# Kernel tuning notes

Measured on AMD Instinct MI355X. Metric: run time of the kernel, lower is better.

The kernel has to match this reference:

```python
import jax, jax.numpy as jnp
import numpy as np

D = 128
H = 128  # scorer hidden

def setup_inputs() -> dict:
    key = jax.random.key(0)
    ks = jax.random.split(key, 8)
    B, T = 4096, 200
    transformer_out = jax.random.normal(ks[0], (B, T, D), dtype=jnp.float32)
    candidate = jax.random.normal(ks[1], (B, D), dtype=jnp.float32)
    mask = jax.random.randint(ks[2], (B, T), 0, 2).astype(jnp.bool_)
    # scorer params: Linear(3D,H) -> PReLU -> Linear(H,1)
    lim1 = 1.0 / np.sqrt(3 * D)
    W1 = jax.random.uniform(ks[3], (3 * D, H), minval=-lim1, maxval=lim1, dtype=jnp.float32)
    b1 = jax.random.uniform(ks[4], (H,), minval=-lim1, maxval=lim1, dtype=jnp.float32)
    a = jnp.array(0.25, dtype=jnp.float32)  # PReLU default init
    lim2 = 1.0 / np.sqrt(H)
    W2 = jax.random.uniform(ks[5], (H, 1), minval=-lim2, maxval=lim2, dtype=jnp.float32)
    b2 = jax.random.uniform(ks[6], (1,), minval=-lim2, maxval=lim2, dtype=jnp.float32)
    return {"transformer_out": transformer_out, "candidate": candidate, "mask": mask,
            "W1": W1, "b1": b1, "a": a, "W2": W2, "b2": b2}

def reference(transformer_out, candidate, mask, W1, b1, a, W2, b2):
    # transformer_out: [B,T,D], candidate: [B,D]
    cand_exp = jnp.broadcast_to(candidate[:, None, :], transformer_out.shape)  # [B,T,D]
    att_input = jnp.concatenate([transformer_out, cand_exp, transformer_out * cand_exp], axis=-1)  # [B,T,3D]
    h = att_input @ W1 + b1                       # [B,T,H]
    h = jnp.where(h >= 0, h, a * h)               # PReLU (single shared alpha)
    scores = (h @ W2 + b2)[..., 0]                # [B,T]
    scores = jnp.where(mask, scores, -jnp.inf)
    weights = jax.nn.softmax(scores, axis=-1)     # [B,T]
    return jnp.einsum('bt,btd->bd', weights, transformer_out)  # [B,D]
```

## Files before the change

kernel.cpp:

```cpp
#include <hip/hip_runtime.h>
#include <hip/hip_bf16.h>

typedef __attribute__((ext_vector_type(8))) short short8;
typedef __attribute__((ext_vector_type(4))) float f32x4;

#define B_T 200
#define B_D 128

static __device__ __forceinline__ short f2bf(float f) {
  unsigned u = __builtin_bit_cast(unsigned, f);
  u += 0x7fffu + ((u >> 16) & 1u);
  return (short)(u >> 16);
}
static __device__ __forceinline__ short8 cvt8(f32x4 a, f32x4 b) {
  short8 t;
  t[0] = f2bf(a[0]); t[1] = f2bf(a[1]); t[2] = f2bf(a[2]); t[3] = f2bf(a[3]);
  t[4] = f2bf(b[0]); t[5] = f2bf(b[1]); t[6] = f2bf(b[2]); t[7] = f2bf(b[3]);
  return t;
}

__global__ __launch_bounds__(256, 4)
void ta_fused(const float* __restrict__ x,
              const float* __restrict__ cand,
              const void*  __restrict__ maskp,
              const float* __restrict__ W1,
              const float* __restrict__ b1,
              const float* __restrict__ ap,
              const float* __restrict__ W2,
              const float* __restrict__ b2p,
              float* __restrict__ out)
{
  __shared__ __align__(16) short wbt[B_D * B_D];
  __shared__ __align__(16) float part[8][B_D];
  __shared__ float w2_lds[B_D];
  __shared__ float scores[208];
  __shared__ float red[8];

  const int b    = blockIdx.x;
  const int tid  = threadIdx.x;
  const int lane = tid & 63;
  const int wv   = tid >> 6;
  const int l15  = lane & 15;
  const int g    = lane >> 4;

  int flag1b;
  {
    const unsigned char* mb = (const unsigned char*)maskp;
    unsigned long long v8 = *(const unsigned long long*)(mb + lane * 8);
    flag1b = __any((v8 & 0xFFFFFF00FFFFFF00ull) != 0ull);
  }
  bool mk = false;
  if (tid < B_T) {
    if (flag1b) mk = ((const unsigned char*)maskp)[(size_t)b * B_T + tid] != 0;
    else        mk = ((const int*)maskp)[(size_t)b * B_T + tid] != 0;
  }

  if (tid < B_D) w2_lds[tid] = W2[tid];

  const float* cb = cand + (size_t)b * B_D;
  {
    const int j = tid & 127;
    const int h = tid >> 7;
    #pragma unroll 2
    for (int it = 0; it < 8; ++it) {
      const int ko = it * 2 + h;
      const int k0 = ko * 8;
      short8 t;
      #pragma unroll
      for (int e = 0; e < 8; ++e) {
        float c  = cb[k0 + e];
        float wa = W1[(size_t)(k0 + e) * B_D + j];
        float wc = W1[(size_t)(256 + k0 + e) * B_D + j];
        t[e] = f2bf(wa + c * wc);
      }
      *(short8*)&wbt[(ko * B_D + j) * 8] = t;
    }
    float s0 = (h == 0) ? b1[j] : 0.f, s1 = 0.f, s2 = 0.f, s3 = 0.f;
    const float* w1b = W1 + (size_t)(B_D + h * 64) * B_D + j;
    #pragma unroll 8
    for (int k = 0; k < 64; k += 4) {
      s0 = fmaf(cb[h * 64 + k    ], w1b[(size_t)(k    ) * B_D], s0);
      s1 = fmaf(cb[h * 64 + k + 1], w1b[(size_t)(k + 1) * B_D], s1);
      s2 = fmaf(cb[h * 64 + k + 2], w1b[(size_t)(k + 2) * B_D], s2);
      s3 = fmaf(cb[h * 64 + k + 3], w1b[(size_t)(k + 3) * B_D], s3);
    }
    part[h][j] = (s0 + s1) + (s2 + s3);
  }
  __syncthreads();

  float betaL[8], w2L[8];
  #pragma unroll
  for (int nt = 0; nt < 8; ++nt) {
    int col = nt * 16 + l15;
    betaL[nt] = part[0][col] + part[1][col];
    w2L[nt]   = w2_lds[col];
  }
  const float alpha = ap[0];

#define TILE_SCORE(MT) do {                                                   \
    int row = (MT) * 16 + l15; if (row > B_T - 1) row = B_T - 1;              \
    const float* xr = x + ((size_t)b * B_T + row) * B_D + g * 8;              \
    f32x4 p0 = *(const f32x4*)(xr +  0), p1 = *(const f32x4*)(xr +   4);      \
    f32x4 p2 = *(const f32x4*)(xr + 32), p3 = *(const f32x4*)(xr +  36);      \
    f32x4 p4 = *(const f32x4*)(xr + 64), p5 = *(const f32x4*)(xr +  68);      \
    f32x4 p6 = *(const f32x4*)(xr + 96), p7 = *(const f32x4*)(xr + 100);      \
    short8 a0 = cvt8(p0, p1), a1 = cvt8(p2, p3);                              \
    short8 a2 = cvt8(p4, p5), a3 = cvt8(p6, p7);                              \
    float sc[4] = {0.f, 0.f, 0.f, 0.f};                                       \
    _Pragma("unroll")                                                         \
    for (int nt = 0; nt < 8; ++nt) {                                          \
      f32x4 acc = {0.f, 0.f, 0.f, 0.f};                                       \
      const short8* wp = (const short8*)wbt + g * B_D + nt * 16 + l15;        \
      acc = __builtin_amdgcn_mfma_f32_16x16x32_bf16(a0, wp[0],    acc, 0,0,0);\
      acc = __builtin_amdgcn_mfma_f32_16x16x32_bf16(a1, wp[512],  acc, 0,0,0);\
      acc = __builtin_amdgcn_mfma_f32_16x16x32_bf16(a2, wp[1024], acc, 0,0,0);\
      acc = __builtin_amdgcn_mfma_f32_16x16x32_bf16(a3, wp[1536], acc, 0,0,0);\
      _Pragma("unroll")                                                       \
      for (int r = 0; r < 4; ++r) {                                           \
        float h = acc[r] + betaL[nt];                                         \
        float p = (h >= 0.f) ? h : alpha * h;                                 \
        sc[r] += p * w2L[nt];                                                 \
      }                                                                       \
    }                                                                         \
    _Pragma("unroll")                                                         \
    for (int r = 0; r < 4; ++r) {                                             \
      float v = sc[r];                                                        \
      v += __shfl_xor(v, 1, 16); v += __shfl_xor(v, 2, 16);                   \
      v += __shfl_xor(v, 4, 16); v += __shfl_xor(v, 8, 16);                   \
      if (l15 == 0) scores[(MT) * 16 + g * 4 + r] = v;                        \
    }                                                                         \
  } while (0)

  TILE_SCORE(wv);
  TILE_SCORE(4 + wv);
  TILE_SCORE(8 + wv);
  if (wv == 0) TILE_SCORE(12);
#undef TILE_SCORE
  __syncthreads();

  {
    float s = (tid < B_T && mk) ? scores[tid] : -INFINITY;
    float v = s;
    #pragma unroll
    for (int m = 32; m >= 1; m >>= 1) v = fmaxf(v, __shfl_xor(v, m, 64));
    if (lane == 0) red[wv] = v;
    __syncthreads();
    float mx = fmaxf(fmaxf(red[0], red[1]), fmaxf(red[2], red[3]));
    float e = mk ? __expf(s - mx) : 0.f;
    float sv = e;
    #pragma unroll
    for (int m = 32; m >= 1; m >>= 1) sv += __shfl_xor(sv, m, 64);
    if (lane == 0) red[4 + wv] = sv;
    if (tid < 208) scores[tid] = e;
    __syncthreads();
  }

  {
    const int d4 = (tid & 31) << 2;
    const int p  = tid >> 5;
    const float* xc = x + ((size_t)b * B_T + p * 25) * B_D + d4;
    f32x4 acc = {0.f, 0.f, 0.f, 0.f};
    #pragma unroll 5
    for (int t = 0; t < 25; ++t) {
      f32x4 xv = *(const f32x4*)(xc + (size_t)t * B_D);
      float w = scores[p * 25 + t];
      acc[0] = fmaf(w, xv[0], acc[0]);
      acc[1] = fmaf(w, xv[1], acc[1]);
      acc[2] = fmaf(w, xv[2], acc[2]);
      acc[3] = fmaf(w, xv[3], acc[3]);
    }
    __syncthreads();
    *(f32x4*)&part[p][d4] = acc;
  }
  __syncthreads();
  if (tid < B_D) {
    float Z = (red[4] + red[5]) + (red[6] + red[7]);
    float s = 0.f;
    #pragma unroll
    for (int p = 0; p < 8; ++p) s += part[p][tid];
    out[(size_t)b * B_D + tid] = s / Z;
  }
}

extern "C" void kernel_launch(void* const* d_in, const int* in_sizes, int n_in,
                              void* d_out, int out_size, void* d_ws, size_t ws_size,
                              hipStream_t stream) {
  const float* x    = (const float*)d_in[0];
  const float* cand = (const float*)d_in[1];
  const void*  mask = d_in[2];
  const float* W1   = (const float*)d_in[3];
  const float* b1   = (const float*)d_in[4];
  const float* a    = (const float*)d_in[5];
  const float* W2   = (const float*)d_in[6];
  const float* b2   = (const float*)d_in[7];
  float* out = (float*)d_out;
  const int B = in_sizes[1] / B_D;
  ta_fused<<<B, 256, 0, stream>>>(x, cand, mask, W1, b1, a, W2, b2, out);
}
```

Measured before the change: 147.7 us.

## Precompute bf16 W1 fragments and per-batch beta in prep kernels

Adds two prep kernels. One converts the W1 x-part and product-part to bf16 fragments in workspace. The other computes beta = b1 + cand·W1_mid for all batches using an LDS-cached W1 slice. The fused kernel then reads half-size bf16 weight fragments with coalesced 16-byte loads and reads beta directly, instead of re-reading fp32 W1 strided per block. It also aliases the partial-sum buffer onto the weight LDS region, shrinking LDS use, and drops one barrier. The cost is two extra launches and a double bf16 rounding of the folded weights.

```diff
diff --git a/kernel.cpp b/kernel.cpp
--- a/kernel.cpp
+++ b/kernel.cpp
@@ -11,12 +11,62 @@
   unsigned u = __builtin_bit_cast(unsigned, f);
   u += 0x7fffu + ((u >> 16) & 1u);
   return (short)(u >> 16);
+}
+static __device__ __forceinline__ float bf2f(short s) {
+  unsigned u = ((unsigned)(unsigned short)s) << 16;
+  return __builtin_bit_cast(float, u);
 }
 static __device__ __forceinline__ short8 cvt8(f32x4 a, f32x4 b) {
   short8 t;
   t[0] = f2bf(a[0]); t[1] = f2bf(a[1]); t[2] = f2bf(a[2]); t[3] = f2bf(a[3]);
   t[4] = f2bf(b[0]); t[5] = f2bf(b[1]); t[6] = f2bf(b[2]); t[7] = f2bf(b[3]);
   return t;
+}
+
+__global__ __launch_bounds__(256) void ta_prep_w(const float* __restrict__ W1,
+                                                 short* __restrict__ wfrag) {
+  const int o = blockIdx.x * 256 + threadIdx.x;
+  const int j = o & 127, k0 = (o >> 7) * 8;
+  short8 ta, tc;
+  #pragma unroll
+  for (int e = 0; e < 8; ++e) {
+    ta[e] = f2bf(W1[(size_t)(k0 + e) * B_D + j]);
+    tc[e] = f2bf(W1[(size_t)(256 + k0 + e) * B_D + j]);
+  }
+  *(short8*)&wfrag[o * 8] = ta;
+  *(short8*)&wfrag[16384 + o * 8] = tc;
+}
+
+__global__ __launch_bounds__(256) void ta_prep_beta(const float* __restrict__ cand,
+                                                    const float* __restrict__ W1,
+                                                    const float* __restrict__ b1,
+                                                    float* __restrict__ beta, int B) {
+  __shared__ float w1b[B_D][B_D];
+  const int tid = threadIdx.x;
+  #pragma unroll
+  for (int i = 0; i < 16; ++i) {
+    int v = i * 256 + tid;
+    ((f32x4*)w1b)[v] = ((const f32x4*)(W1 + 128 * B_D))[v];
+  }
+  __syncthreads();
+  const int j = tid & 127, which = tid >> 7;
+  const int b0 = blockIdx.x * 8;
+  #pragma unroll
+  for (int bi = 0; bi < 4; ++bi) {
+    int b = b0 + bi * 2 + which;
+    if (b < B) {
+      const float* cb = cand + (size_t)b * B_D;
+      float s0 = b1[j], s1 = 0.f, s2 = 0.f, s3 = 0.f;
+      #pragma unroll 8
+      for (int k = 0; k < 128; k += 4) {
+        s0 = fmaf(cb[k    ], w1b[k    ][j], s0);
+        s1 = fmaf(cb[k + 1], w1b[k + 1][j], s1);
+        s2 = fmaf(cb[k + 2], w1b[k + 2][j], s2);
+        s3 = fmaf(cb[k + 3], w1b[k + 3][j], s3);
+      }
+      beta[(size_t)b * B_D + j] = (s0 + s1) + (s2 + s3);
+    }
+  }
 }
 
 __global__ __launch_bounds__(256, 4)
@@ -27,14 +77,17 @@
               const float* __restrict__ b1,
               const float* __restrict__ ap,
               const float* __restrict__ W2,
-              const float* __restrict__ b2p,
+              const short* __restrict__ wfrag,
+              const float* __restrict__ beta,
+              int use_ws,
               float* __restrict__ out)
 {
   __shared__ __align__(16) short wbt[B_D * B_D];
-  __shared__ __align__(16) float part[8][B_D];
+  __shared__ float bpart[2][B_D];
   __shared__ float w2_lds[B_D];
   __shared__ float scores[208];
   __shared__ float red[8];
+  float (*part)[B_D] = (float (*)[B_D])wbt;
 
   const int b    = blockIdx.x;
   const int tid  = threadIdx.x;
@@ -58,20 +111,31 @@
   if (tid < B_D) w2_lds[tid] = W2[tid];
 
   const float* cb = cand + (size_t)b * B_D;
-  {
-    const int j = tid & 127;
-    const int h = tid >> 7;
+  if (use_ws) {
     #pragma unroll 2
     for (int it = 0; it < 8; ++it) {
-      const int ko = it * 2 + h;
-      const int k0 = ko * 8;
+      const int o = it * 256 + tid;
+      const int k0 = (o >> 7) * 8;
+      short8 wa = *(const short8*)&wfrag[o * 8];
+      short8 wc = *(const short8*)&wfrag[16384 + o * 8];
+      short8 t;
+      #pragma unroll
+      for (int e = 0; e < 8; ++e)
+        t[e] = f2bf(fmaf(cb[k0 + e], bf2f(wc[e]), bf2f(wa[e])));
+      *(short8*)&wbt[o * 8] = t;
+    }
+  } else {
+    const int j = tid & 127, h = tid >> 7;
+    #pragma unroll 2
+    for (int it = 0; it < 8; ++it) {
+      const int ko = it * 2 + h, k0 = ko * 8;
       short8 t;
       #pragma unroll
       for (int e = 0; e < 8; ++e) {
         float c  = cb[k0 + e];
         float wa = W1[(size_t)(k0 + e) * B_D + j];
         float wc = W1[(size_t)(256 + k0 + e) * B_D + j];
-        t[e] = f2bf(wa + c * wc);
+        t[e] = f2bf(fmaf(c, wc, wa));
       }
       *(short8*)&wbt[(ko * B_D + j) * 8] = t;
     }
@@ -84,7 +148,7 @@
       s2 = fmaf(cb[h * 64 + k + 2], w1b[(size_t)(k + 2) * B_D], s2);
       s3 = fmaf(cb[h * 64 + k + 3], w1b[(size_t)(k + 3) * B_D], s3);
     }
-    part[h][j] = (s0 + s1) + (s2 + s3);
+    bpart[h][j] = (s0 + s1) + (s2 + s3);
   }
   __syncthreads();
 
@@ -92,7 +156,7 @@
   #pragma unroll
   for (int nt = 0; nt < 8; ++nt) {
     int col = nt * 16 + l15;
-    betaL[nt] = part[0][col] + part[1][col];
+    betaL[nt] = use_ws ? beta[(size_t)b * B_D + col] : (bpart[0][col] + bpart[1][col]);
     w2L[nt]   = w2_lds[col];
   }
   const float alpha = ap[0];
@@ -169,7 +233,6 @@
       acc[2] = fmaf(w, xv[2], acc[2]);
       acc[3] = fmaf(w, xv[3], acc[3]);
     }
-    __syncthreads();
     *(f32x4*)&part[p][d4] = acc;
   }
   __syncthreads();
@@ -192,8 +255,18 @@
   const float* b1   = (const float*)d_in[4];
   const float* a    = (const float*)d_in[5];
   const float* W2   = (const float*)d_in[6];
-  const float* b2   = (const float*)d_in[7];
   float* out = (float*)d_out;
   const int B = in_sizes[1] / B_D;
-  ta_fused<<<B, 256, 0, stream>>>(x, cand, mask, W1, b1, a, W2, b2, out);
-}
+
+  short* wfrag = (short*)d_ws;
+  float* beta  = (float*)((char*)d_ws + 65536);
+  const size_t need = 65536 + (size_t)B * B_D * sizeof(float);
+  const int use_ws = (ws_size >= need) ? 1 : 0;
+
+  if (use_ws) {
+    ta_prep_w<<<8, 256, 0, stream>>>(W1, wfrag);
+    ta_prep_beta<<<(B + 7) / 8, 256, 0, stream>>>(cand, W1, b1, beta, B);
+  }
+  ta_fused<<<B, 256, 0, stream>>>(x, cand, mask, W1, b1, a, W2,
+                                  wfrag, beta, use_ws, out);
+}
```

New measurement: 152.1 us. 3.0% more time.

## Prefetch x tiles ahead of MFMA scoring and overlap first load with W1 fold

Applied to the files above, without the earlier changes.

Loads the first row tile of x at kernel entry so its latency overlaps the weight-folding prologue. Later tiles are prefetched into registers before computing the current tile's scores. Also reads W2 directly instead of staging it in LDS, uses two accumulators in the weighted pooling loop, and drops a redundant barrier. Occupancy hints change to an explicit waves-per-EU attribute. This raises register pressure in exchange for hiding memory latency.

```diff
diff --git a/kernel.cpp b/kernel.cpp
--- a/kernel.cpp
+++ b/kernel.cpp
@@ -19,7 +19,8 @@
   return t;
 }
 
-__global__ __launch_bounds__(256, 4)
+__global__ __launch_bounds__(256)
+__attribute__((amdgpu_waves_per_eu(4, 4)))
 void ta_fused(const float* __restrict__ x,
               const float* __restrict__ cand,
               const void*  __restrict__ maskp,
@@ -31,8 +32,7 @@
               float* __restrict__ out)
 {
   __shared__ __align__(16) short wbt[B_D * B_D];
-  __shared__ __align__(16) float part[8][B_D];
-  __shared__ float w2_lds[B_D];
+  __shared__ float part[8][B_D];
   __shared__ float scores[208];
   __shared__ float red[8];
 
@@ -43,6 +43,12 @@
   const int l15  = lane & 15;
   const int g    = lane >> 4;
 
+  const float* xr0p = x + ((size_t)b * B_T + wv * 16 + l15) * B_D + g * 8;
+  f32x4 r0 = *(const f32x4*)(xr0p +  0), r1 = *(const f32x4*)(xr0p +   4);
+  f32x4 r2 = *(const f32x4*)(xr0p + 32), r3 = *(const f32x4*)(xr0p +  36);
+  f32x4 r4 = *(const f32x4*)(xr0p + 64), r5 = *(const f32x4*)(xr0p +  68);
+  f32x4 r6 = *(const f32x4*)(xr0p + 96), r7 = *(const f32x4*)(xr0p + 100);
+
   int flag1b;
   {
     const unsigned char* mb = (const unsigned char*)maskp;
@@ -55,23 +61,20 @@
     else        mk = ((const int*)maskp)[(size_t)b * B_T + tid] != 0;
   }
 
-  if (tid < B_D) w2_lds[tid] = W2[tid];
-
   const float* cb = cand + (size_t)b * B_D;
   {
     const int j = tid & 127;
     const int h = tid >> 7;
     #pragma unroll 2
     for (int it = 0; it < 8; ++it) {
-      const int ko = it * 2 + h;
-      const int k0 = ko * 8;
+      const int ko = it * 2 + h, k0 = ko * 8;
       short8 t;
       #pragma unroll
       for (int e = 0; e < 8; ++e) {
         float c  = cb[k0 + e];
         float wa = W1[(size_t)(k0 + e) * B_D + j];
         float wc = W1[(size_t)(256 + k0 + e) * B_D + j];
-        t[e] = f2bf(wa + c * wc);
+        t[e] = f2bf(fmaf(c, wc, wa));
       }
       *(short8*)&wbt[(ko * B_D + j) * 8] = t;
     }
@@ -93,19 +96,19 @@
   for (int nt = 0; nt < 8; ++nt) {
     int col = nt * 16 + l15;
     betaL[nt] = part[0][col] + part[1][col];
-    w2L[nt]   = w2_lds[col];
+    w2L[nt]   = W2[col];
   }
   const float alpha = ap[0];
 
-#define TILE_SCORE(MT) do {                                                   \
-    int row = (MT) * 16 + l15; if (row > B_T - 1) row = B_T - 1;              \
-    const float* xr = x + ((size_t)b * B_T + row) * B_D + g * 8;              \
-    f32x4 p0 = *(const f32x4*)(xr +  0), p1 = *(const f32x4*)(xr +   4);      \
-    f32x4 p2 = *(const f32x4*)(xr + 32), p3 = *(const f32x4*)(xr +  36);      \
-    f32x4 p4 = *(const f32x4*)(xr + 64), p5 = *(const f32x4*)(xr +  68);      \
-    f32x4 p6 = *(const f32x4*)(xr + 96), p7 = *(const f32x4*)(xr + 100);      \
-    short8 a0 = cvt8(p0, p1), a1 = cvt8(p2, p3);                              \
-    short8 a2 = cvt8(p4, p5), a3 = cvt8(p6, p7);                              \
+#define LOADX(MT_ROW) do {                                                    \
+    const float* xp_ = x + ((size_t)b * B_T + (MT_ROW)) * B_D + g * 8;        \
+    r0 = *(const f32x4*)(xp_ +  0); r1 = *(const f32x4*)(xp_ +   4);          \
+    r2 = *(const f32x4*)(xp_ + 32); r3 = *(const f32x4*)(xp_ +  36);          \
+    r4 = *(const f32x4*)(xp_ + 64); r5 = *(const f32x4*)(xp_ +  68);          \
+    r6 = *(const f32x4*)(xp_ + 96); r7 = *(const f32x4*)(xp_ + 100);          \
+  } while (0)
+
+#define COMPUTE_SCORE(TB) do {                                                \
     float sc[4] = {0.f, 0.f, 0.f, 0.f};                                       \
     _Pragma("unroll")                                                         \
     for (int nt = 0; nt < 8; ++nt) {                                          \
@@ -117,9 +120,9 @@
       acc = __builtin_amdgcn_mfma_f32_16x16x32_bf16(a3, wp[1536], acc, 0,0,0);\
       _Pragma("unroll")                                                       \
       for (int r = 0; r < 4; ++r) {                                           \
-        float h = acc[r] + betaL[nt];                                         \
-        float p = (h >= 0.f) ? h : alpha * h;                                 \
-        sc[r] += p * w2L[nt];                                                 \
+        float h_ = acc[r] + betaL[nt];                                        \
+        float p_ = (h_ >= 0.f) ? h_ : alpha * h_;                             \
+        sc[r] += p_ * w2L[nt];                                                \
       }                                                                       \
     }                                                                         \
     _Pragma("unroll")                                                         \
@@ -127,15 +130,31 @@
       float v = sc[r];                                                        \
       v += __shfl_xor(v, 1, 16); v += __shfl_xor(v, 2, 16);                   \
       v += __shfl_xor(v, 4, 16); v += __shfl_xor(v, 8, 16);                   \
-      if (l15 == 0) scores[(MT) * 16 + g * 4 + r] = v;                        \
+      if (l15 == 0) scores[(TB) + g * 4 + r] = v;                             \
     }                                                                         \
   } while (0)
 
-  TILE_SCORE(wv);
-  TILE_SCORE(4 + wv);
-  TILE_SCORE(8 + wv);
-  if (wv == 0) TILE_SCORE(12);
-#undef TILE_SCORE
+  short8 a0 = cvt8(r0, r1), a1 = cvt8(r2, r3), a2 = cvt8(r4, r5), a3 = cvt8(r6, r7);
+  LOADX((4 + wv) * 16 + l15);
+  COMPUTE_SCORE(wv * 16);
+
+  a0 = cvt8(r0, r1); a1 = cvt8(r2, r3); a2 = cvt8(r4, r5); a3 = cvt8(r6, r7);
+  LOADX((8 + wv) * 16 + l15);
+  COMPUTE_SCORE((4 + wv) * 16);
+
+  a0 = cvt8(r0, r1); a1 = cvt8(r2, r3); a2 = cvt8(r4, r5); a3 = cvt8(r6, r7);
+  if (wv == 0) {
+    int row3 = 192 + l15; if (row3 > B_T - 1) row3 = B_T - 1;
+    LOADX(row3);
+  }
+  COMPUTE_SCORE((8 + wv) * 16);
+
+  if (wv == 0) {
+    a0 = cvt8(r0, r1); a1 = cvt8(r2, r3); a2 = cvt8(r4, r5); a3 = cvt8(r6, r7);
+    COMPUTE_SCORE(192);
+  }
+#undef LOADX
+#undef COMPUTE_SCORE
   __syncthreads();
 
   {
@@ -159,18 +178,26 @@
     const int d4 = (tid & 31) << 2;
     const int p  = tid >> 5;
     const float* xc = x + ((size_t)b * B_T + p * 25) * B_D + d4;
-    f32x4 acc = {0.f, 0.f, 0.f, 0.f};
-    #pragma unroll 5
-    for (int t = 0; t < 25; ++t) {
-      f32x4 xv = *(const f32x4*)(xc + (size_t)t * B_D);
-      float w = scores[p * 25 + t];
-      acc[0] = fmaf(w, xv[0], acc[0]);
-      acc[1] = fmaf(w, xv[1], acc[1]);
-      acc[2] = fmaf(w, xv[2], acc[2]);
-      acc[3] = fmaf(w, xv[3], acc[3]);
-    }
-    __syncthreads();
-    *(f32x4*)&part[p][d4] = acc;
+    f32x4 acc0 = {0.f, 0.f, 0.f, 0.f}, acc1 = {0.f, 0.f, 0.f, 0.f};
+    #pragma unroll
+    for (int t = 0; t < 24; t += 2) {
+      f32x4 xv0 = *(const f32x4*)(xc + (size_t)t * B_D);
+      f32x4 xv1 = *(const f32x4*)(xc + (size_t)(t + 1) * B_D);
+      float w0 = scores[p * 25 + t];
+      float w1 = scores[p * 25 + t + 1];
+      acc0[0] = fmaf(w0, xv0[0], acc0[0]); acc1[0] = fmaf(w1, xv1[0], acc1[0]);
+      acc0[1] = fmaf(w0, xv0[1], acc0[1]); acc1[1] = fmaf(w1, xv1[1], acc1[1]);
+      acc0[2] = fmaf(w0, xv0[2], acc0[2]); acc1[2] = fmaf(w1, xv1[2], acc1[2]);
+      acc0[3] = fmaf(w0, xv0[3], acc0[3]); acc1[3] = fmaf(w1, xv1[3], acc1[3]);
+    }
+    {
+      f32x4 xv = *(const f32x4*)(xc + (size_t)24 * B_D);
+      float w = scores[p * 25 + 24];
+      acc0[0] = fmaf(w, xv[0], acc0[0]); acc0[1] = fmaf(w, xv[1], acc0[1]);
+      acc0[2] = fmaf(w, xv[2], acc0[2]); acc0[3] = fmaf(w, xv[3], acc0[3]);
+    }
+    acc0[0] += acc1[0]; acc0[1] += acc1[1]; acc0[2] += acc1[2]; acc0[3] += acc1[3];
+    *(f32x4*)&part[p][d4] = acc0;
   }
   __syncthreads();
   if (tid < B_D) {
```

After: 147.5 us. About the same (-0.1%).

## Split each batch row across two blocks with a split-softmax combine kernel

Applied to the files above, without the earlier changes.

Each batch row's 200 timesteps are split between two blocks. Each block computes a local max, normalizer and unnormalized weighted sum into workspace, and a second kernel rescales and merges the two halves. This halves per-block scoring and pooling work to raise parallelism, but every block still rebuilds the fused bf16 weight tile and bias from W1, so that setup cost is duplicated and a second launch is added. LDS is also reduced by aliasing the partial-sum buffer onto the weight tile and reading W2 directly from global memory.

```diff
diff --git a/kernel.cpp b/kernel.cpp
--- a/kernel.cpp
+++ b/kernel.cpp
@@ -20,23 +20,30 @@
 }
 
 __global__ __launch_bounds__(256, 4)
-void ta_fused(const float* __restrict__ x,
-              const float* __restrict__ cand,
-              const void*  __restrict__ maskp,
-              const float* __restrict__ W1,
-              const float* __restrict__ b1,
-              const float* __restrict__ ap,
-              const float* __restrict__ W2,
-              const float* __restrict__ b2p,
-              float* __restrict__ out)
+void ta_half(const float* __restrict__ x,
+             const float* __restrict__ cand,
+             const void*  __restrict__ maskp,
+             const float* __restrict__ W1,
+             const float* __restrict__ b1,
+             const float* __restrict__ ap,
+             const float* __restrict__ W2,
+             float* __restrict__ wsO,
+             float* __restrict__ wsMZ)
 {
   __shared__ __align__(16) short wbt[B_D * B_D];
-  __shared__ __align__(16) float part[8][B_D];
-  __shared__ float w2_lds[B_D];
-  __shared__ float scores[208];
+  __shared__ float bpart[2][B_D];
+  __shared__ float scores[112];
   __shared__ float red[8];
-
-  const int b    = blockIdx.x;
+  float (*part)[B_D] = (float (*)[B_D])wbt;
+
+  const int bi   = blockIdx.x;
+  const int b    = bi >> 1;
+  const int half = bi & 1;
+  const int mt0  = half ? 7 : 0;
+  const int NT   = half ? 6 : 7;
+  const int L    = NT * 16;
+  const int rbase = mt0 * 16;
+
   const int tid  = threadIdx.x;
   const int lane = tid & 63;
   const int wv   = tid >> 6;
@@ -50,12 +57,13 @@
     flag1b = __any((v8 & 0xFFFFFF00FFFFFF00ull) != 0ull);
   }
   bool mk = false;
-  if (tid < B_T) {
-    if (flag1b) mk = ((const unsigned char*)maskp)[(size_t)b * B_T + tid] != 0;
-    else        mk = ((const int*)maskp)[(size_t)b * B_T + tid] != 0;
-  }
-
-  if (tid < B_D) w2_lds[tid] = W2[tid];
+  {
+    const int grow = rbase + tid;
+    if (tid < L && grow < B_T) {
+      if (flag1b) mk = ((const unsigned char*)maskp)[(size_t)b * B_T + grow] != 0;
+      else        mk = ((const int*)maskp)[(size_t)b * B_T + grow] != 0;
+    }
+  }
 
   const float* cb = cand + (size_t)b * B_D;
   {
@@ -63,15 +71,14 @@
     const int h = tid >> 7;
     #pragma unroll 2
     for (int it = 0; it < 8; ++it) {
-      const int ko = it * 2 + h;
-      const int k0 = ko * 8;
+      const int ko = it * 2 + h, k0 = ko * 8;
       short8 t;
       #pragma unroll
       for (int e = 0; e < 8; ++e) {
         float c  = cb[k0 + e];
         float wa = W1[(size_t)(k0 + e) * B_D + j];
         float wc = W1[(size_t)(256 + k0 + e) * B_D + j];
-        t[e] = f2bf(wa + c * wc);
+        t[e] = f2bf(fmaf(c, wc, wa));
       }
       *(short8*)&wbt[(ko * B_D + j) * 8] = t;
     }
@@ -84,7 +91,7 @@
       s2 = fmaf(cb[h * 64 + k + 2], w1b[(size_t)(k + 2) * B_D], s2);
       s3 = fmaf(cb[h * 64 + k + 3], w1b[(size_t)(k + 3) * B_D], s3);
     }
-    part[h][j] = (s0 + s1) + (s2 + s3);
+    bpart[h][j] = (s0 + s1) + (s2 + s3);
   }
   __syncthreads();
 
@@ -92,8 +99,8 @@
   #pragma unroll
   for (int nt = 0; nt < 8; ++nt) {
     int col = nt * 16 + l15;
-    betaL[nt] = part[0][col] + part[1][col];
-    w2L[nt]   = w2_lds[col];
+    betaL[nt] = bpart[0][col] + bpart[1][col];
+    w2L[nt]   = W2[col];
   }
   const float alpha = ap[0];
 
@@ -117,9 +124,9 @@
       acc = __builtin_amdgcn_mfma_f32_16x16x32_bf16(a3, wp[1536], acc, 0,0,0);\
       _Pragma("unroll")                                                       \
       for (int r = 0; r < 4; ++r) {                                           \
-        float h = acc[r] + betaL[nt];                                         \
-        float p = (h >= 0.f) ? h : alpha * h;                                 \
-        sc[r] += p * w2L[nt];                                                 \
+        float h_ = acc[r] + betaL[nt];                                        \
+        float p_ = (h_ >= 0.f) ? h_ : alpha * h_;                             \
+        sc[r] += p_ * w2L[nt];                                                \
       }                                                                       \
     }                                                                         \
     _Pragma("unroll")                                                         \
@@ -127,59 +134,79 @@
       float v = sc[r];                                                        \
       v += __shfl_xor(v, 1, 16); v += __shfl_xor(v, 2, 16);                   \
       v += __shfl_xor(v, 4, 16); v += __shfl_xor(v, 8, 16);                   \
-      if (l15 == 0) scores[(MT) * 16 + g * 4 + r] = v;                        \
+      if (l15 == 0) scores[((MT) - mt0) * 16 + g * 4 + r] = v;                \
     }                                                                         \
   } while (0)
 
-  TILE_SCORE(wv);
-  TILE_SCORE(4 + wv);
-  TILE_SCORE(8 + wv);
-  if (wv == 0) TILE_SCORE(12);
+  TILE_SCORE(mt0 + wv);
+  if (wv + 4 < NT) TILE_SCORE(mt0 + 4 + wv);
 #undef TILE_SCORE
   __syncthreads();
 
-  {
-    float s = (tid < B_T && mk) ? scores[tid] : -INFINITY;
+  float mloc, Zloc;
+  {
+    float s = (tid < L && mk) ? scores[tid] : -INFINITY;
     float v = s;
     #pragma unroll
     for (int m = 32; m >= 1; m >>= 1) v = fmaxf(v, __shfl_xor(v, m, 64));
     if (lane == 0) red[wv] = v;
     __syncthreads();
-    float mx = fmaxf(fmaxf(red[0], red[1]), fmaxf(red[2], red[3]));
-    float e = mk ? __expf(s - mx) : 0.f;
+    mloc = fmaxf(fmaxf(red[0], red[1]), fmaxf(red[2], red[3]));
+    float e = (tid < L && mk) ? __expf(s - mloc) : 0.f;
     float sv = e;
     #pragma unroll
     for (int m = 32; m >= 1; m >>= 1) sv += __shfl_xor(sv, m, 64);
     if (lane == 0) red[4 + wv] = sv;
-    if (tid < 208) scores[tid] = e;
+    if (tid < L) scores[tid] = e;
     __syncthreads();
+    Zloc = (red[4] + red[5]) + (red[6] + red[7]);
   }
 
   {
     const int d4 = (tid & 31) << 2;
     const int p  = tid >> 5;
-    const float* xc = x + ((size_t)b * B_T + p * 25) * B_D + d4;
-    f32x4 acc = {0.f, 0.f, 0.f, 0.f};
-    #pragma unroll 5
-    for (int t = 0; t < 25; ++t) {
-      f32x4 xv = *(const f32x4*)(xc + (size_t)t * B_D);
-      float w = scores[p * 25 + t];
-      acc[0] = fmaf(w, xv[0], acc[0]);
-      acc[1] = fmaf(w, xv[1], acc[1]);
-      acc[2] = fmaf(w, xv[2], acc[2]);
-      acc[3] = fmaf(w, xv[3], acc[3]);
-    }
-    __syncthreads();
-    *(f32x4*)&part[p][d4] = acc;
+    const int nt = L >> 3;
+    const float* xb = x + (size_t)b * B_T * B_D + d4;
+    f32x4 acc0 = {0.f, 0.f, 0.f, 0.f}, acc1 = {0.f, 0.f, 0.f, 0.f};
+    #pragma unroll 6
+    for (int t = 0; t < nt; t += 2) {
+      int r0 = rbase + p * nt + t;     if (r0 > B_T - 1) r0 = B_T - 1;
+      int r1 = rbase + p * nt + t + 1; if (r1 > B_T - 1) r1 = B_T - 1;
+      f32x4 xv0 = *(const f32x4*)(xb + (size_t)r0 * B_D);
+      f32x4 xv1 = *(const f32x4*)(xb + (size_t)r1 * B_D);
+      float w0 = scores[p * nt + t];
+      float w1 = scores[p * nt + t + 1];
+      acc0[0] = fmaf(w0, xv0[0], acc0[0]); acc1[0] = fmaf(w1, xv1[0], acc1[0]);
+      acc0[1] = fmaf(w0, xv0[1], acc0[1]); acc1[1] = fmaf(w1, xv1[1], acc1[1]);
+      acc0[2] = fmaf(w0, xv0[2], acc0[2]); acc1[2] = fmaf(w1, xv1[2], acc1[2]);
+      acc0[3] = fmaf(w0, xv0[3], acc0[3]); acc1[3] = fmaf(w1, xv1[3], acc1[3]);
+    }
+    acc0[0] += acc1[0]; acc0[1] += acc1[1]; acc0[2] += acc1[2]; acc0[3] += acc1[3];
+    *(f32x4*)&part[p][d4] = acc0;
   }
   __syncthreads();
   if (tid < B_D) {
-    float Z = (red[4] + red[5]) + (red[6] + red[7]);
     float s = 0.f;
     #pragma unroll
     for (int p = 0; p < 8; ++p) s += part[p][tid];
-    out[(size_t)b * B_D + tid] = s / Z;
-  }
+    wsO[(size_t)bi * B_D + tid] = s;
+  }
+  if (tid == 0) { wsMZ[bi * 2] = mloc; wsMZ[bi * 2 + 1] = Zloc; }
+}
+
+__global__ __launch_bounds__(128)
+void ta_combine(const float* __restrict__ wsO, const float* __restrict__ wsMZ,
+                float* __restrict__ out) {
+  const int b = blockIdx.x, d = threadIdx.x;
+  const float m1 = wsMZ[(b * 2    ) * 2], Z1 = wsMZ[(b * 2    ) * 2 + 1];
+  const float m2 = wsMZ[(b * 2 + 1) * 2], Z2 = wsMZ[(b * 2 + 1) * 2 + 1];
+  const float m  = fmaxf(m1, m2);
+  const float f1 = (Z1 > 0.f) ? __expf(m1 - m) : 0.f;
+  const float f2 = (Z2 > 0.f) ? __expf(m2 - m) : 0.f;
+  const float Z  = f1 * Z1 + f2 * Z2;
+  const float o1 = wsO[(size_t)(b * 2) * B_D + d];
+  const float o2 = wsO[(size_t)(b * 2 + 1) * B_D + d];
+  out[(size_t)b * B_D + d] = (f1 * o1 + f2 * o2) / Z;
 }
 
 extern "C" void kernel_launch(void* const* d_in, const int* in_sizes, int n_in,
@@ -192,8 +219,12 @@
   const float* b1   = (const float*)d_in[4];
   const float* a    = (const float*)d_in[5];
   const float* W2   = (const float*)d_in[6];
-  const float* b2   = (const float*)d_in[7];
   float* out = (float*)d_out;
   const int B = in_sizes[1] / B_D;
-  ta_fused<<<B, 256, 0, stream>>>(x, cand, mask, W1, b1, a, W2, b2, out);
-}
+
+  float* wsO  = (float*)d_ws;
+  float* wsMZ = (float*)((char*)d_ws + (size_t)B * 2 * B_D * 4);
+
+  ta_half<<<B * 2, 256, 0, stream>>>(x, cand, mask, W1, b1, a, W2, wsO, wsMZ);
+  ta_combine<<<B, 128, 0, stream>>>(wsO, wsMZ, out);
+}
```

Measured after the change: 185.8 us. 25.8% more time.
